# Kernel tuning notes

Hardware: AMD Instinct MI355X
Metric: run time of the kernel (lower is better)

## Reference

```python
import jax, jax.numpy as jnp
import numpy as np

N_LAYERS = 2        # f_aux_layer_num
DIM = 512           # aux_dim
HEADS = 8           # aux_attn_num
HEAD = DIM // HEADS # 64 == aux_attn_dim
FFN_H = int(DIM * 2.0)  # ffn_factor = 2.0 -> 1024
BLOCK = 64          # f_block_size n
L_BLOCKS = 32
M = BLOCK + 1       # block + router token
EPS = 1e-5
THETA = 10000.0


def rms_norm(x, w):
    return x * jax.lax.rsqrt(jnp.mean(x * x, axis=-1, keepdims=True) + EPS) * w


def rotary(x):
    # x: [b, h, s, a]; matches RotaryEmb: halves rotated with outer(t, inv_freq)
    s, a = x.shape[2], x.shape[3]
    inv_freq = (1.0 / THETA) ** (jnp.arange(0, a, 2, dtype=jnp.float32) / a)
    freqs = jnp.arange(s, dtype=jnp.float32)[:, None] * inv_freq[None, :]  # [s, a/2]
    cos, sin = jnp.cos(freqs), jnp.sin(freqs)
    x1, x2 = jnp.split(x, 2, axis=-1)
    return jnp.concatenate([x1 * cos + x2 * sin, -x1 * sin + x2 * cos], axis=-1)


def setup_inputs() -> dict:
    key = jax.random.key(0)
    ks = jax.random.split(key, 10)
    B = 2
    S = L_BLOCKS * M
    x = jax.random.normal(ks[0], (B, L_BLOCKS * BLOCK, DIM), jnp.float32)
    doc = jnp.sort(jax.random.randint(ks[1], (B, S), 0, 4, dtype=jnp.int32), axis=-1)
    w = 0.02
    return {
        "x": x,
        "doc": doc,
        "router_token": jax.random.normal(ks[2], (DIM,), jnp.float32),
        "attn_w": jax.random.normal(ks[3], (N_LAYERS, DIM, 3 * DIM), jnp.float32) * w,
        "attn_o_w": jax.random.normal(ks[4], (N_LAYERS, DIM, DIM), jnp.float32) * w,
        "ffn_up_w": jax.random.normal(ks[5], (N_LAYERS, DIM, 2 * FFN_H), jnp.float32) * w,
        "ffn_down_w": jax.random.normal(ks[6], (N_LAYERS, FFN_H, DIM), jnp.float32) * w,
        "attn_norm_w": jnp.ones((N_LAYERS, DIM), jnp.float32),
        "ffn_norm_w": jnp.ones((N_LAYERS, DIM), jnp.float32),
    }


def reference(x, doc, router_token, attn_w, attn_o_w, ffn_up_w, ffn_down_w,
              attn_norm_w, ffn_norm_w):
    b = x.shape[0]
    # insert router token after each block: [b, l, n+1, d] -> [b, s, d]
    xb = x.reshape(b, L_BLOCKS, BLOCK, DIM)
    rt = jnp.broadcast_to(router_token, (b, L_BLOCKS, 1, DIM))
    h = jnp.concatenate([xb, rt], axis=2).reshape(b, L_BLOCKS * M, DIM)
    s = h.shape[1]

    # mask_mod_1: block-causal AND same-doc
    blk = jnp.arange(s) // M
    causal = blk[:, None] >= blk[None, :]                       # [s, s]
    mask = causal[None] & (doc[:, :, None] == doc[:, None, :])  # [b, s, s]
    neg = jnp.finfo(h.dtype).min
    scale = 1.0 / jnp.sqrt(jnp.float32(HEAD))

    def split_heads(t):
        return t.reshape(b, s, HEADS, HEAD).transpose(0, 2, 1, 3)

    for i in range(N_LAYERS):
        hn = rms_norm(h, attn_norm_w[i])
        qkv = hn @ attn_w[i]                       # [b, s, 3*dim]
        q, k, v = jnp.split(qkv, 3, axis=-1)
        q, k, v = split_heads(q), split_heads(k), split_heads(v)
        q, k = rotary(q), rotary(k)
        scores = jnp.einsum('bhqa,bhka->bhqk', q, k) * scale
        scores = jnp.where(mask[:, None], scores, neg)
        attn = jax.nn.softmax(scores, axis=-1)
        o = jnp.einsum('bhqk,bhka->bhqa', attn, v)
        o = o.transpose(0, 2, 1, 3).reshape(b, s, DIM)
        h = h + o @ attn_o_w[i]
        hf = rms_norm(h, ffn_norm_w[i])
        u1, u2 = jnp.split(hf @ ffn_up_w[i], 2, axis=-1)
        h = h + (jax.nn.silu(u1) * u2) @ ffn_down_w[i]

    # keep router-token slot of each block: [b, l, d]
    return h.reshape(b, L_BLOCKS, M, DIM)[:, :, -1]
```

## Files before the change

kernel.cpp:

```cpp
#include <hip/hip_runtime.h>
#include <math.h>

#define NB 2
#define LB 32
#define BLKN 64
#define MM 65
#define SS (LB*MM)
#define DD 512
#define NH 8
#define HD 64
#define FFH 1024
#define ROWS (NB*SS)
#define WT_LS 2621440

typedef __attribute__((ext_vector_type(8))) short bf16x8;
typedef __attribute__((ext_vector_type(4))) float f32x4;

__device__ __forceinline__ unsigned short f2bf(float f) {
    union { float f; unsigned u; } v; v.f = f;
    unsigned r = (v.u + 0x7FFFu + ((v.u >> 16) & 1u)) >> 16;
    return (unsigned short)r;
}
__device__ __forceinline__ float bf2f(unsigned short u) {
    union { unsigned u; float f; } v; v.u = ((unsigned)u) << 16; return v.f;
}

__device__ __forceinline__ void gload_lds16(const unsigned short* g, unsigned short* l) {
    __builtin_amdgcn_global_load_lds((const __attribute__((address_space(1))) unsigned int*)g,
                                     (__attribute__((address_space(3))) unsigned int*)l,
                                     16, 0, 0);
}

__device__ __forceinline__ int grow_map(int r) {
    return (r >> 5) * SS + (r & 31) * MM + BLKN;
}

template <int FIRST>
__global__ __launch_bounds__(256) void rms4_k(const float* __restrict__ hsrc,
                                              const float* __restrict__ x,
                                              const float* __restrict__ rt,
                                              const float* __restrict__ w,
                                              float* __restrict__ hout,
                                              unsigned short* __restrict__ out) {
    int row = blockIdx.x * 4 + (threadIdx.x >> 6);
    int lane = threadIdx.x & 63;
    const float* sp;
    if (FIRST) {
        int s = row % SS, b = row / SS;
        int l = s / MM, j = s % MM;
        sp = (j < BLKN) ? x + ((size_t)(b * LB + l) * BLKN + j) * DD : rt;
    } else {
        sp = hsrc + (size_t)row * DD;
    }
    float4 a = *(const float4*)(sp + lane * 8);
    float4 bq = *(const float4*)(sp + lane * 8 + 4);
    float ss = a.x * a.x + a.y * a.y + a.z * a.z + a.w * a.w
             + bq.x * bq.x + bq.y * bq.y + bq.z * bq.z + bq.w * bq.w;
    #pragma unroll
    for (int off = 32; off; off >>= 1) ss += __shfl_xor(ss, off);
    float r = rsqrtf(ss * (1.0f / 512.0f) + 1e-5f);
    float4 w0 = *(const float4*)(w + lane * 8);
    float4 w1 = *(const float4*)(w + lane * 8 + 4);
    unsigned short o8[8] = {f2bf(a.x * r * w0.x), f2bf(a.y * r * w0.y),
                            f2bf(a.z * r * w0.z), f2bf(a.w * r * w0.w),
                            f2bf(bq.x * r * w1.x), f2bf(bq.y * r * w1.y),
                            f2bf(bq.z * r * w1.z), f2bf(bq.w * r * w1.w)};
    *(bf16x8*)(out + (size_t)row * DD + lane * 8) = *(const bf16x8*)o8;
    if (FIRST) {
        *(float4*)(hout + (size_t)row * DD + lane * 8) = a;
        *(float4*)(hout + (size_t)row * DD + lane * 8 + 4) = bq;
    }
}

__global__ __launch_bounds__(256) void wtrans_all_k(const float* __restrict__ attn_w,
                                                    const float* __restrict__ attn_o_w,
                                                    const float* __restrict__ up_w,
                                                    const float* __restrict__ down_w,
                                                    unsigned short* __restrict__ wt) {
    __shared__ unsigned short T[64][66];
    int wg = blockIdx.x;
    int layer = wg >= 640;
    int r = wg - layer * 640;
    const float* W; int K, N; size_t dstOff; int perm = 0;
    if (r < 192)      { W = attn_w   + (size_t)layer * 512 * 1536; K = 512;  N = 1536; dstOff = 0; }
    else if (r < 256) { W = attn_o_w + (size_t)layer * 512 * 512;  K = 512;  N = 512;  dstOff = 786432;  r -= 192; }
    else if (r < 512) { W = up_w     + (size_t)layer * 512 * 2048; K = 512;  N = 2048; dstOff = 1048576; perm = 1; r -= 256; }
    else              { W = down_w   + (size_t)layer * 1024 * 512; K = 1024; N = 512;  dstOff = 2097152; r -= 512; }
    unsigned short* dst = wt + (size_t)layer * WT_LS + dstOff;
    int ntn = N >> 6;
    int n0 = (r % ntn) * 64, k0 = (r / ntn) * 64;
    int t = threadIdx.x;
    #pragma unroll
    for (int i = 0; i < 16; ++i) {
        int e = t + i * 256;
        int rr = e >> 6, cc = e & 63;
        T[rr][cc] = f2bf(W[(size_t)(k0 + rr) * N + n0 + cc]);
    }
    __syncthreads();
    #pragma unroll
    for (int i = 0; i < 16; ++i) {
        int e = t + i * 256;
        int rr = e >> 6, cc = e & 63;
        int n = n0 + rr;
        int nr = n;
        if (perm) {
            int p = n & 1023;
            nr = ((p >> 4) << 5) | ((n >> 10) << 4) | (p & 15);
        }
        dst[(size_t)nr * K + k0 + cc] = T[cc][rr];
    }
}

template <int ADD, int OBF, int ROPE, int SILU>
__global__ __launch_bounds__(256) void gemm128_k(const unsigned short* __restrict__ A,
                                                 const unsigned short* __restrict__ Wt,
                                                 void* __restrict__ Cp,
                                                 int K, int N, int colOff) {
    __shared__ unsigned short As[128 * 64];
    __shared__ unsigned short Bs[128 * 64];
    int t = threadIdx.x;
    int lane = t & 63, wv = t >> 6;
    int wm = wv >> 1, wn = wv & 1;
    int rowBase = blockIdx.y * 128, colBase = blockIdx.x * 128;
    int c = lane & 15, g = lane >> 4;
    int sw = (c & 7) << 4;

    f32x4 acc[4][4];
    #pragma unroll
    for (int mt = 0; mt < 4; ++mt)
        #pragma unroll
        for (int nt = 0; nt < 4; ++nt) { f32x4 z = {0, 0, 0, 0}; acc[mt][nt] = z; }

    for (int k0 = 0; k0 < K; k0 += 64) {
        __syncthreads();
        #pragma unroll
        for (int i = 0; i < 4; ++i) {
            int e0 = (i * 4 + wv) * 64;
            int e = e0 + lane;
            int row = e >> 3;
            int kb = ((e & 7) << 4) ^ ((row & 7) << 4);
            int gr = rowBase + row; if (gr > ROWS - 1) gr = ROWS - 1;
            gload_lds16(A + (size_t)gr * K + k0 + (kb >> 1), &As[e0 * 8]);
        }
        #pragma unroll
        for (int i = 0; i < 4; ++i) {
            int e0 = (i * 4 + wv) * 64;
            int e = e0 + lane;
            int row = e >> 3;
            int kb = ((e & 7) << 4) ^ ((row & 7) << 4);
            gload_lds16(Wt + (size_t)(colOff + colBase + row) * K + k0 + (kb >> 1), &Bs[e0 * 8]);
        }
        __syncthreads();

        bf16x8 af[4][2], bfr[4][2];
        #pragma unroll
        for (int mt = 0; mt < 4; ++mt)
            #pragma unroll
            for (int hf = 0; hf < 2; ++hf)
                af[mt][hf] = *(const bf16x8*)
                    &As[((wm * 64 + mt * 16 + c) * 128 + ((hf * 64 + g * 16) ^ sw)) >> 1];
        #pragma unroll
        for (int nt = 0; nt < 4; ++nt)
            #pragma unroll
            for (int hf = 0; hf < 2; ++hf)
                bfr[nt][hf] = *(const bf16x8*)
                    &Bs[((wn * 64 + nt * 16 + c) * 128 + ((hf * 64 + g * 16) ^ sw)) >> 1];
        __builtin_amdgcn_s_setprio(1);
        #pragma unroll
        for (int mt = 0; mt < 4; ++mt)
            #pragma unroll
            for (int nt = 0; nt < 4; ++nt) {
                acc[mt][nt] = __builtin_amdgcn_mfma_f32_16x16x32_bf16(af[mt][0], bfr[nt][0], acc[mt][nt], 0, 0, 0);
                acc[mt][nt] = __builtin_amdgcn_mfma_f32_16x16x32_bf16(af[mt][1], bfr[nt][1], acc[mt][nt], 0, 0, 0);
            }
        __builtin_amdgcn_s_setprio(0);
    }

    if (ROPE) {
        int sec = (colOff + colBase + wn * 64) >> 9;
        if (sec < 2) {
            #pragma unroll
            for (int mt = 0; mt < 4; ++mt)
                #pragma unroll
                for (int j = 0; j < 4; ++j) {
                    int row = rowBase + wm * 64 + mt * 16 + g * 4 + j;
                    int spos = row % SS;
                    #pragma unroll
                    for (int p = 0; p < 2; ++p) {
                        float jj = (float)(c + p * 16);
                        float inv = exp2f(jj * -0.41524101186092030f);
                        float fr = (float)spos * inv;
                        float sn, cs; __sincosf(fr, &sn, &cs);
                        float a = acc[mt][p][j], bb = acc[mt][p + 2][j];
                        acc[mt][p][j] = a * cs + bb * sn;
                        acc[mt][p + 2][j] = -a * sn + bb * cs;
                    }
                }
        }
    }

    #pragma unroll
    for (int mt = 0; mt < 4; ++mt)
        #pragma unroll
        for (int j = 0; j < 4; ++j) {
            int row = rowBase + wm * 64 + mt * 16 + g * 4 + j;
            if (row >= ROWS) continue;
            if (SILU) {
                unsigned short* gr = (unsigned short*)Cp + (size_t)row * 1024;
                #pragma unroll
                for (int ntp = 0; ntp < 2; ++ntp) {
                    int npr = colBase + wn * 64 + ntp * 32;
                    int p = ((npr >> 5) << 4) + c;
                    float u1 = acc[mt][2 * ntp][j];
                    float u2 = acc[mt][2 * ntp + 1][j];
                    gr[p] = f2bf((u1 / (1.0f + __expf(-u1))) * u2);
                }
            } else {
                size_t off = (size_t)row * N + colOff + colBase + wn * 64 + c;
                if (OBF) {
                    unsigned short* cr = (unsigned short*)Cp + off;
                    #pragma unroll
                    for (int nt = 0; nt < 4; ++nt) cr[nt * 16] = f2bf(acc[mt][nt][j]);
                } else {
                    float* cr = (float*)Cp + off;
                    #pragma unroll
                    for (int nt = 0; nt < 4; ++nt) {
                        if (ADD) cr[nt * 16] += acc[mt][nt][j];
                        else     cr[nt * 16] = acc[mt][nt][j];
                    }
                }
            }
        }
}

template <int MODE, int ADD>
__global__ __launch_bounds__(256) void gemm64_k(const unsigned short* __restrict__ A,
                                                const unsigned short* __restrict__ Wt,
                                                void* __restrict__ Cp,
                                                const float* __restrict__ Hsrc,
                                                float* __restrict__ outp,
                                                int K, int N) {
    __shared__ unsigned short As[64 * 64];
    __shared__ unsigned short Bs[128 * 64];
    int t = threadIdx.x;
    int lane = t & 63, wv = t >> 6;
    int wm = wv >> 1, wn = wv & 1;
    int rowBase = blockIdx.y * 64, colBase = blockIdx.x * 128;
    int c = lane & 15, g = lane >> 4;
    int sw = (c & 7) << 4;

    f32x4 acc[2][4];
    #pragma unroll
    for (int mt = 0; mt < 2; ++mt)
        #pragma unroll
        for (int nt = 0; nt < 4; ++nt) { f32x4 z = {0, 0, 0, 0}; acc[mt][nt] = z; }

    for (int k0 = 0; k0 < K; k0 += 64) {
        __syncthreads();
        #pragma unroll
        for (int i = 0; i < 2; ++i) {
            int e0 = (i * 4 + wv) * 64;
            int e = e0 + lane;
            int row = e >> 3;
            int kb = ((e & 7) << 4) ^ ((row & 7) << 4);
            int gr = rowBase + row;
            gload_lds16(A + (size_t)gr * K + k0 + (kb >> 1), &As[e0 * 8]);
        }
        #pragma unroll
        for (int i = 0; i < 4; ++i) {
            int e0 = (i * 4 + wv) * 64;
            int e = e0 + lane;
            int row = e >> 3;
            int kb = ((e & 7) << 4) ^ ((row & 7) << 4);
            gload_lds16(Wt + (size_t)(colBase + row) * K + k0 + (kb >> 1), &Bs[e0 * 8]);
        }
        __syncthreads();

        bf16x8 af[2][2], bfr[4][2];
        #pragma unroll
        for (int mt = 0; mt < 2; ++mt)
            #pragma unroll
            for (int hf = 0; hf < 2; ++hf)
                af[mt][hf] = *(const bf16x8*)
                    &As[((wm * 32 + mt * 16 + c) * 128 + ((hf * 64 + g * 16) ^ sw)) >> 1];
        #pragma unroll
        for (int nt = 0; nt < 4; ++nt)
            #pragma unroll
            for (int hf = 0; hf < 2; ++hf)
                bfr[nt][hf] = *(const bf16x8*)
                    &Bs[((wn * 64 + nt * 16 + c) * 128 + ((hf * 64 + g * 16) ^ sw)) >> 1];
        __builtin_amdgcn_s_setprio(1);
        #pragma unroll
        for (int mt = 0; mt < 2; ++mt)
            #pragma unroll
            for (int nt = 0; nt < 4; ++nt) {
                acc[mt][nt] = __builtin_amdgcn_mfma_f32_16x16x32_bf16(af[mt][0], bfr[nt][0], acc[mt][nt], 0, 0, 0);
                acc[mt][nt] = __builtin_amdgcn_mfma_f32_16x16x32_bf16(af[mt][1], bfr[nt][1], acc[mt][nt], 0, 0, 0);
            }
        __builtin_amdgcn_s_setprio(0);
    }

    #pragma unroll
    for (int mt = 0; mt < 2; ++mt)
        #pragma unroll
        for (int j = 0; j < 4; ++j) {
            int row = rowBase + wm * 32 + mt * 16 + g * 4 + j;
            int col = colBase + wn * 64 + c;
            if (MODE == 0) {
                float* cr = (float*)Cp + (size_t)row * N + col;
                #pragma unroll
                for (int nt = 0; nt < 4; ++nt) {
                    if (ADD) cr[nt * 16] += acc[mt][nt][j];
                    else     cr[nt * 16] = acc[mt][nt][j];
                }
            } else if (MODE == 2) {
                int gr = grow_map(row);
                float* cr = (float*)Cp + (size_t)row * 512 + col;
                const float* hsr = Hsrc + (size_t)gr * 512 + col;
                #pragma unroll
                for (int nt = 0; nt < 4; ++nt) cr[nt * 16] = hsr[nt * 16] + acc[mt][nt][j];
            } else if (MODE == 3) {
                float* cr = outp + (size_t)row * 512 + col;
                const float* hsr = Hsrc + (size_t)row * 512 + col;
                #pragma unroll
                for (int nt = 0; nt < 4; ++nt) cr[nt * 16] = hsr[nt * 16] + acc[mt][nt][j];
            } else {
                unsigned short* gr = (unsigned short*)Cp + (size_t)row * 1024;
                #pragma unroll
                for (int ntp = 0; ntp < 2; ++ntp) {
                    int npr = colBase + wn * 64 + ntp * 32;
                    int p = ((npr >> 5) << 4) + c;
                    float u1 = acc[mt][2 * ntp][j];
                    float u2 = acc[mt][2 * ntp + 1][j];
                    gr[p] = f2bf((u1 / (1.0f + __expf(-u1))) * u2);
                }
            }
        }
}

#define QR 80

__global__ __launch_bounds__(320) void attn_mfma_k(const unsigned short* __restrict__ qkv,
                                                   const int* __restrict__ doc,
                                                   unsigned short* __restrict__ o) {
    __shared__ unsigned short Qs[QR * 64];
    __shared__ unsigned short Ks[2][64 * 64];
    __shared__ unsigned short Vt[2][64][72];
    __shared__ unsigned short Ps[5][16][72];
    __shared__ int docq[QR];
    __shared__ int dock[2][64];

    int idx = blockIdx.x;
    int l = 31 - (idx >> 4);
    int b = (idx >> 3) & 1;
    int h = idx & 7;
    int t = threadIdx.x;
    int lane = t & 63;
    int wv = t >> 6;

    const unsigned short* qb = qkv + (size_t)b * SS * 1536;
    int rowq0 = l * MM;
    int kmax = (l + 1) * MM;

    #pragma unroll
    for (int it = 0; it < 2; ++it) {
        int ebase = it * 320 + wv * 64;
        int e = ebase + lane;
        int row = e >> 3;
        int kb = ((e & 7) << 4) ^ ((row & 7) << 4);
        int gr = rowq0 + row; if (gr > SS - 1) gr = SS - 1;
        gload_lds16(qb + (size_t)gr * 1536 + h * 64 + (kb >> 1), &Qs[ebase * 8]);
    }
    if (t < QR) docq[t] = (t < MM) ? doc[b * SS + rowq0 + t] : -999999;

    int d0 = doc[b * SS + rowq0];
    int lo = 0, hi = rowq0;
    while (lo < hi) {
        int mid = (lo + hi) >> 1;
        if (doc[b * SS + mid] < d0) lo = mid + 1; else hi = mid;
    }
    int kts = lo >> 6;
    int nkt = (kmax + 63) >> 6;

    const int mt = wv;
    const int g = lane >> 4;
    const int c = lane & 15;
    const int sw = (c & 7) << 4;

    auto stageK = [&](int kbase, int buf) {
        int ebase = wv * 64;
        int e = ebase + lane;
        int row = e >> 3;
        int kb = ((e & 7) << 4) ^ ((row & 7) << 4);
        int kg = kbase + row; if (kg > kmax - 1) kg = kmax - 1;
        gload_lds16(qb + (size_t)kg * 1536 + 512 + h * 64 + (kb >> 1), &Ks[buf][ebase * 8]);
        if (wv < 3) {
            int eb2 = 320 + wv * 64;
            int e2 = eb2 + lane;
            int row2 = e2 >> 3;
            int kb2 = ((e2 & 7) << 4) ^ ((row2 & 7) << 4);
            int kg2 = kbase + row2; if (kg2 > kmax - 1) kg2 = kmax - 1;
            gload_lds16(qb + (size_t)kg2 * 1536 + 512 + h * 64 + (kb2 >> 1), &Ks[buf][eb2 * 8]);
        }
    };
    bf16x8 vr0, vr1; int dnx = 0;
    auto loadV = [&](int kbase) {
        int key = t & 63;
        int de = (t >> 6) * 8;
        int kg = kbase + key; if (kg > kmax - 1) kg = kmax - 1;
        vr0 = *(const bf16x8*)(qb + (size_t)kg * 1536 + 1024 + h * 64 + de);
        if (t < 192) {
            int e2 = 320 + t;
            int key2 = e2 & 63;
            int de2 = (e2 >> 6) * 8;
            int kg2 = kbase + key2; if (kg2 > kmax - 1) kg2 = kmax - 1;
            vr1 = *(const bf16x8*)(qb + (size_t)kg2 * 1536 + 1024 + h * 64 + de2);
        }
        if (t < 64) dnx = (kbase + t < kmax) ? doc[b * SS + kbase + t] : -1000000;
    };
    auto writeV = [&](int buf) {
        int key = t & 63;
        int de = (t >> 6) * 8;
        #pragma unroll
        for (int jj = 0; jj < 8; ++jj) Vt[buf][de + jj][key] = ((unsigned short*)&vr0)[jj];
        if (t < 192) {
            int e2 = 320 + t;
            int key2 = e2 & 63;
            int de2 = (e2 >> 6) * 8;
            #pragma unroll
            for (int jj = 0; jj < 8; ++jj) Vt[buf][de2 + jj][key2] = ((unsigned short*)&vr1)[jj];
        }
        if (t < 64) dock[buf][t] = dnx;
    };

    stageK(kts << 6, 0);
    loadV(kts << 6);
    writeV(0);
    __syncthreads();

    bf16x8 aq[2];
    #pragma unroll
    for (int hf = 0; hf < 2; ++hf)
        aq[hf] = *(const bf16x8*)&Qs[((mt * 16 + c) * 128 + ((hf * 64 + g * 16) ^ sw)) >> 1];
    int dq[4];
    #pragma unroll
    for (int j = 0; j < 4; ++j) dq[j] = docq[mt * 16 + g * 4 + j];

    f32x4 oacc[4];
    float m_[4], l_[4];
    #pragma unroll
    for (int nt = 0; nt < 4; ++nt) { f32x4 z = {0,0,0,0}; oacc[nt] = z; }
    #pragma unroll
    for (int j = 0; j < 4; ++j) { m_[j] = -1e30f; l_[j] = 0.0f; }

    for (int kt = kts; kt < nkt; ++kt) {
        int cur = (kt - kts) & 1;
        bool more = (kt + 1 < nkt);
        if (more) {
            stageK((kt + 1) << 6, cur ^ 1);
            loadV((kt + 1) << 6);
        }

        f32x4 s[4];
        __builtin_amdgcn_s_setprio(1);
        #pragma unroll
        for (int sub = 0; sub < 4; ++sub) {
            f32x4 acc = {0, 0, 0, 0};
            #pragma unroll
            for (int hf = 0; hf < 2; ++hf) {
                bf16x8 bk = *(const bf16x8*)
                    &Ks[cur][((sub * 16 + c) * 128 + ((hf * 64 + g * 16) ^ sw)) >> 1];
                acc = __builtin_amdgcn_mfma_f32_16x16x32_bf16(aq[hf], bk, acc, 0, 0, 0);
            }
            s[sub] = acc;
        }
        __builtin_amdgcn_s_setprio(0);
        #pragma unroll
        for (int sub = 0; sub < 4; ++sub) {
            int dk = dock[cur][sub * 16 + c];
            #pragma unroll
            for (int j = 0; j < 4; ++j)
                s[sub][j] = (dq[j] == dk) ? s[sub][j] * 0.125f : -1e30f;
        }
        float mx[4];
        #pragma unroll
        for (int j = 0; j < 4; ++j)
            mx[j] = fmaxf(fmaxf(s[0][j], s[1][j]), fmaxf(s[2][j], s[3][j]));
        #pragma unroll
        for (int off = 1; off < 16; off <<= 1)
            #pragma unroll
            for (int j = 0; j < 4; ++j) mx[j] = fmaxf(mx[j], __shfl_xor(mx[j], off));
        float mn[4], sc[4], rs[4];
        #pragma unroll
        for (int j = 0; j < 4; ++j) {
            mn[j] = fmaxf(m_[j], mx[j]);
            sc[j] = __expf(m_[j] - mn[j]);
            m_[j] = mn[j];
            rs[j] = 0.0f;
        }
        #pragma unroll
        for (int sub = 0; sub < 4; ++sub)
            #pragma unroll
            for (int j = 0; j < 4; ++j) {
                float p = __expf(s[sub][j] - mn[j]);
                rs[j] += p;
                Ps[wv][g * 4 + j][sub * 16 + c] = f2bf(p);
            }
        #pragma unroll
        for (int off = 1; off < 16; off <<= 1)
            #pragma unroll
            for (int j = 0; j < 4; ++j) rs[j] += __shfl_xor(rs[j], off);
        #pragma unroll
        for (int j = 0; j < 4; ++j) l_[j] = l_[j] * sc[j] + rs[j];
        #pragma unroll
        for (int nt = 0; nt < 4; ++nt)
            #pragma unroll
            for (int j = 0; j < 4; ++j) oacc[nt][j] *= sc[j];
        __builtin_amdgcn_s_setprio(1);
        #pragma unroll
        for (int hf = 0; hf < 2; ++hf) {
            bf16x8 af = *(const bf16x8*)&Ps[wv][c][hf * 32 + g * 8];
            #pragma unroll
            for (int nt = 0; nt < 4; ++nt) {
                bf16x8 bv = *(const bf16x8*)&Vt[cur][nt * 16 + c][hf * 32 + g * 8];
                oacc[nt] = __builtin_amdgcn_mfma_f32_16x16x32_bf16(af, bv, oacc[nt], 0, 0, 0);
            }
        }
        __builtin_amdgcn_s_setprio(0);

        if (more) writeV(cur ^ 1);
        __syncthreads();
    }

    #pragma unroll
    for (int j = 0; j < 4; ++j) {
        int row = mt * 16 + g * 4 + j;
        if (row < MM) {
            float invl = 1.0f / l_[j];
            #pragma unroll
            for (int nt = 0; nt < 4; ++nt)
                o[(size_t)(b * SS + rowq0 + row) * DD + h * 64 + nt * 16 + c] =
                    f2bf(oacc[nt][j] * invl);
        }
    }
}

__global__ __launch_bounds__(256) void rattn_k(const unsigned short* __restrict__ hnb,
                                               const unsigned short* __restrict__ qkv,
                                               const unsigned short* __restrict__ wq,
                                               const int* __restrict__ doc,
                                               unsigned short* __restrict__ obr) {
    __shared__ float hn_r[DD];
    __shared__ float qs[HD];
    __shared__ float sc[SS];
    __shared__ float red_m[4], red_s[4];
    __shared__ float pacc[4][HD];

    int idx = blockIdx.x;
    int b = idx >> 8, h = (idx >> 5) & 7, l = idx & 31;
    int t = threadIdx.x;
    int lane = t & 63, wv = t >> 6;

    const unsigned short* qb = qkv + (size_t)b * SS * 1536;
    int spos = l * MM + BLKN;
    int rowq = b * SS + spos;
    int kmax = (l + 1) * MM;

    {
        unsigned v = *(const unsigned*)(hnb + (size_t)rowq * DD + t * 2);
        hn_r[t * 2] = bf2f((unsigned short)(v & 0xffff));
        hn_r[t * 2 + 1] = bf2f((unsigned short)(v >> 16));
    }
    int dr = doc[rowq];
    int lo = 0, hi = spos;
    while (lo < hi) {
        int mid = (lo + hi) >> 1;
        if (doc[b * SS + mid] < dr) lo = mid + 1; else hi = mid;
    }
    __syncthreads();

    {
        float part = 0.0f;
        const unsigned short* wr = wq + (size_t)(h * 64 + lane) * DD + wv * 128;
        #pragma unroll
        for (int k8 = 0; k8 < 16; ++k8) {
            bf16x8 w8 = *(const bf16x8*)(wr + k8 * 8);
            #pragma unroll
            for (int j = 0; j < 8; ++j)
                part += hn_r[wv * 128 + k8 * 8 + j] * bf2f((unsigned short)w8[j]);
        }
        pacc[wv][lane] = part;
    }
    __syncthreads();
    if (wv == 0) {
        float dq = pacc[0][lane] + pacc[1][lane] + pacc[2][lane] + pacc[3][lane];
        float other = __shfl_xor(dq, 32);
        float jj = (float)(lane & 31);
        float inv = exp2f(jj * -0.41524101186092030f);
        float fr = (float)spos * inv;
        float sn, cs; __sincosf(fr, &sn, &cs);
        float q1 = (lane < 32) ? dq : other;
        float q2 = (lane < 32) ? other : dq;
        qs[lane] = (lane < 32) ? (q1 * cs + q2 * sn) : (-q1 * sn + q2 * cs);
    }
    __syncthreads();

    int dc = lane & 7, k8 = lane >> 3;
    float mx = -1e30f;
    for (int k0 = lo; k0 < kmax; k0 += 32) {
        int k = k0 + wv * 8 + k8;
        float d = 0.0f;
        if (k < kmax) {
            bf16x8 kv = *(const bf16x8*)(qb + (size_t)k * 1536 + 512 + h * 64 + dc * 8);
            #pragma unroll
            for (int j = 0; j < 8; ++j)
                d += bf2f((unsigned short)kv[j]) * qs[dc * 8 + j];
        }
        #pragma unroll
        for (int off = 1; off < 8; off <<= 1) d += __shfl_xor(d, off);
        if (k < kmax) {
            float s = d * 0.125f;
            if (dc == 0) sc[k] = s;
            mx = fmaxf(mx, s);
        }
    }
    #pragma unroll
    for (int off = 32; off; off >>= 1) mx = fmaxf(mx, __shfl_xor(mx, off));
    if (lane == 0) red_m[wv] = mx;
    __syncthreads();
    mx = fmaxf(fmaxf(red_m[0], red_m[1]), fmaxf(red_m[2], red_m[3]));

    float sum = 0.0f;
    for (int k = lo + t; k < kmax; k += 256) {
        float p = __expf(sc[k] - mx);
        sc[k] = p;
        sum += p;
    }
    #pragma unroll
    for (int off = 32; off; off >>= 1) sum += __shfl_xor(sum, off);
    if (lane == 0) red_s[wv] = sum;
    __syncthreads();
    sum = red_s[0] + red_s[1] + red_s[2] + red_s[3];

    float acc = 0.0f;
    #pragma unroll 4
    for (int k = lo + wv; k < kmax; k += 4) {
        float vv = bf2f(qb[(size_t)k * 1536 + 1024 + h * 64 + lane]);
        acc += sc[k] * vv;
    }
    pacc[wv][lane] = acc;
    __syncthreads();
    if (wv == 0) {
        float o = (pacc[0][lane] + pacc[1][lane] + pacc[2][lane] + pacc[3][lane]) / sum;
        obr[(size_t)(b * LB + l) * DD + h * 64 + lane] = f2bf(o);
    }
}

extern "C" void kernel_launch(void* const* d_in, const int* in_sizes, int n_in,
                              void* d_out, int out_size, void* d_ws, size_t ws_size,
                              hipStream_t stream) {
    const float* x           = (const float*)d_in[0];
    const int*   doc         = (const int*)d_in[1];
    const float* rt          = (const float*)d_in[2];
    const float* attn_w      = (const float*)d_in[3];
    const float* attn_o_w    = (const float*)d_in[4];
    const float* ffn_up_w    = (const float*)d_in[5];
    const float* ffn_down_w  = (const float*)d_in[6];
    const float* attn_norm_w = (const float*)d_in[7];
    const float* ffn_norm_w  = (const float*)d_in[8];
    float* out = (float*)d_out;

    float* h = (float*)d_ws;
    unsigned short* qkvb = (unsigned short*)(h + (size_t)ROWS * 512);
    unsigned short* wt   = qkvb + (size_t)ROWS * 1536;
    unsigned short* hnb  = wt + (size_t)2 * WT_LS;
    unsigned short* ob   = hnb + (size_t)ROWS * 512;
    unsigned short* gb   = ob + (size_t)ROWS * 512;
    unsigned short* obr  = gb + (size_t)ROWS * 1024;
    unsigned short* hnr  = obr + 64 * 512;
    unsigned short* gbr  = hnr + 64 * 512;
    float* hr = (float*)(gbr + 64 * 1024);

    wtrans_all_k<<<1280, 256, 0, stream>>>(attn_w, attn_o_w, ffn_up_w, ffn_down_w, wt);

    rms4_k<1><<<ROWS / 4, 256, 0, stream>>>(h, x, rt, attn_norm_w, h, hnb);
    gemm128_k<0, 1, 1, 0><<<dim3(12, 33), 256, 0, stream>>>(hnb, wt, qkvb, 512, 1536, 0);
    attn_mfma_k<<<512, 320, 0, stream>>>(qkvb, doc, ob);
    gemm64_k<0, 1><<<dim3(4, 65), 256, 0, stream>>>(ob, wt + 786432, h, nullptr, nullptr, 512, 512);
    rms4_k<0><<<ROWS / 4, 256, 0, stream>>>(h, x, rt, ffn_norm_w, h, hnb);
    gemm128_k<0, 0, 0, 1><<<dim3(16, 33), 256, 0, stream>>>(hnb, wt + 1048576, gb, 512, 2048, 0);
    gemm64_k<0, 1><<<dim3(4, 65), 256, 0, stream>>>(gb, wt + 2097152, h, nullptr, nullptr, 1024, 512);

    unsigned short* wl = wt + (size_t)WT_LS;
    rms4_k<0><<<ROWS / 4, 256, 0, stream>>>(h, x, rt, attn_norm_w + 512, h, hnb);
    gemm128_k<0, 1, 1, 0><<<dim3(8, 33), 256, 0, stream>>>(hnb, wl, qkvb, 512, 1536, 512);
    rattn_k<<<512, 256, 0, stream>>>(hnb, qkvb, wl, doc, obr);
    gemm64_k<2, 0><<<dim3(4, 1), 256, 0, stream>>>(obr, wl + 786432, hr, h, nullptr, 512, 512);
    rms4_k<0><<<16, 256, 0, stream>>>(hr, x, rt, ffn_norm_w + 512, nullptr, hnr);
    gemm64_k<4, 0><<<dim3(16, 1), 256, 0, stream>>>(hnr, wl + 1048576, gbr, nullptr, nullptr, 512, 2048);
    gemm64_k<3, 0><<<dim3(4, 1), 256, 0, stream>>>(gbr, wl + 2097152, nullptr, hr, out, 1024, 512);
}
```

Baseline: 198.9 us.

## Store residual stream in bf16 and unroll router attention PV loop

The fp32 residual buffer h becomes bf16 throughout, in the RMS norm kernels, the GEMM residual-add epilogues and the router path, which halves residual read/write traffic. The attention kernel's block index mapping changes for the second half of the grid, and the router attention's PV accumulation uses four independent accumulators for more ILP. Keeping the residual in bf16 drops precision on the accumulated stream and adds rounding at each residual add, so accuracy could drift.

After: 202.5 us. Within noise of the previous version (+1.8%).

```diff
diff --git a/kernel.cpp b/kernel.cpp
--- a/kernel.cpp
+++ b/kernel.cpp
@@ -36,39 +36,46 @@
 }
 
 template <int FIRST>
-__global__ __launch_bounds__(256) void rms4_k(const float* __restrict__ hsrc,
+__global__ __launch_bounds__(256) void rms4_k(const unsigned short* __restrict__ hsrc,
                                               const float* __restrict__ x,
                                               const float* __restrict__ rt,
                                               const float* __restrict__ w,
-                                              float* __restrict__ hout,
+                                              unsigned short* __restrict__ hout,
                                               unsigned short* __restrict__ out) {
     int row = blockIdx.x * 4 + (threadIdx.x >> 6);
     int lane = threadIdx.x & 63;
-    const float* sp;
+    float v[8];
     if (FIRST) {
         int s = row % SS, b = row / SS;
         int l = s / MM, j = s % MM;
-        sp = (j < BLKN) ? x + ((size_t)(b * LB + l) * BLKN + j) * DD : rt;
+        const float* sp = (j < BLKN) ? x + ((size_t)(b * LB + l) * BLKN + j) * DD : rt;
+        float4 a = *(const float4*)(sp + lane * 8);
+        float4 bq = *(const float4*)(sp + lane * 8 + 4);
+        v[0] = a.x; v[1] = a.y; v[2] = a.z; v[3] = a.w;
+        v[4] = bq.x; v[5] = bq.y; v[6] = bq.z; v[7] = bq.w;
     } else {
-        sp = hsrc + (size_t)row * DD;
-    }
-    float4 a = *(const float4*)(sp + lane * 8);
-    float4 bq = *(const float4*)(sp + lane * 8 + 4);
-    float ss = a.x * a.x + a.y * a.y + a.z * a.z + a.w * a.w
-             + bq.x * bq.x + bq.y * bq.y + bq.z * bq.z + bq.w * bq.w;
+        bf16x8 h8 = *(const bf16x8*)(hsrc + (size_t)row * DD + lane * 8);
+        #pragma unroll
+        for (int j = 0; j < 8; ++j) v[j] = bf2f((unsigned short)h8[j]);
+    }
+    float ss = 0.0f;
+    #pragma unroll
+    for (int j = 0; j < 8; ++j) ss += v[j] * v[j];
     #pragma unroll
     for (int off = 32; off; off >>= 1) ss += __shfl_xor(ss, off);
     float r = rsqrtf(ss * (1.0f / 512.0f) + 1e-5f);
     float4 w0 = *(const float4*)(w + lane * 8);
     float4 w1 = *(const float4*)(w + lane * 8 + 4);
-    unsigned short o8[8] = {f2bf(a.x * r * w0.x), f2bf(a.y * r * w0.y),
-                            f2bf(a.z * r * w0.z), f2bf(a.w * r * w0.w),
-                            f2bf(bq.x * r * w1.x), f2bf(bq.y * r * w1.y),
-                            f2bf(bq.z * r * w1.z), f2bf(bq.w * r * w1.w)};
+    float wv[8] = {w0.x, w0.y, w0.z, w0.w, w1.x, w1.y, w1.z, w1.w};
+    unsigned short o8[8];
+    #pragma unroll
+    for (int j = 0; j < 8; ++j) o8[j] = f2bf(v[j] * r * wv[j]);
     *(bf16x8*)(out + (size_t)row * DD + lane * 8) = *(const bf16x8*)o8;
     if (FIRST) {
-        *(float4*)(hout + (size_t)row * DD + lane * 8) = a;
-        *(float4*)(hout + (size_t)row * DD + lane * 8 + 4) = bq;
+        unsigned short h8[8];
+        #pragma unroll
+        for (int j = 0; j < 8; ++j) h8[j] = f2bf(v[j]);
+        *(bf16x8*)(hout + (size_t)row * DD + lane * 8) = *(const bf16x8*)h8;
     }
 }
 
@@ -237,7 +244,7 @@
 __global__ __launch_bounds__(256) void gemm64_k(const unsigned short* __restrict__ A,
                                                 const unsigned short* __restrict__ Wt,
                                                 void* __restrict__ Cp,
-                                                const float* __restrict__ Hsrc,
+                                                const unsigned short* __restrict__ Hsrc,
                                                 float* __restrict__ outp,
                                                 int K, int N) {
     __shared__ unsigned short As[64 * 64];
@@ -307,23 +314,28 @@
             int row = rowBase + wm * 32 + mt * 16 + g * 4 + j;
             int col = colBase + wn * 64 + c;
             if (MODE == 0) {
-                float* cr = (float*)Cp + (size_t)row * N + col;
-                #pragma unroll
-                for (int nt = 0; nt < 4; ++nt) {
-                    if (ADD) cr[nt * 16] += acc[mt][nt][j];
-                    else     cr[nt * 16] = acc[mt][nt][j];
+                if (ADD) {
+                    unsigned short* cr = (unsigned short*)Cp + (size_t)row * N + col;
+                    #pragma unroll
+                    for (int nt = 0; nt < 4; ++nt)
+                        cr[nt * 16] = f2bf(bf2f(cr[nt * 16]) + acc[mt][nt][j]);
+                } else {
+                    float* cr = (float*)Cp + (size_t)row * N + col;
+                    #pragma unroll
+                    for (int nt = 0; nt < 4; ++nt) cr[nt * 16] = acc[mt][nt][j];
                 }
             } else if (MODE == 2) {
                 int gr = grow_map(row);
-                float* cr = (float*)Cp + (size_t)row * 512 + col;
-                const float* hsr = Hsrc + (size_t)gr * 512 + col;
+                unsigned short* cr = (unsigned short*)Cp + (size_t)row * 512 + col;
+                const unsigned short* hsr = Hsrc + (size_t)gr * 512 + col;
                 #pragma unroll
-                for (int nt = 0; nt < 4; ++nt) cr[nt * 16] = hsr[nt * 16] + acc[mt][nt][j];
+                for (int nt = 0; nt < 4; ++nt)
+                    cr[nt * 16] = f2bf(bf2f(hsr[nt * 16]) + acc[mt][nt][j]);
             } else if (MODE == 3) {
                 float* cr = outp + (size_t)row * 512 + col;
-                const float* hsr = Hsrc + (size_t)row * 512 + col;
+                const unsigned short* hsr = Hsrc + (size_t)row * 512 + col;
                 #pragma unroll
-                for (int nt = 0; nt < 4; ++nt) cr[nt * 16] = hsr[nt * 16] + acc[mt][nt][j];
+                for (int nt = 0; nt < 4; ++nt) cr[nt * 16] = bf2f(hsr[nt * 16]) + acc[mt][nt][j];
             } else {
                 unsigned short* gr = (unsigned short*)Cp + (size_t)row * 1024;
                 #pragma unroll
@@ -351,7 +363,7 @@
     __shared__ int dock[2][64];
 
     int idx = blockIdx.x;
-    int l = 31 - (idx >> 4);
+    int l = (idx < 256) ? (31 - (idx >> 4)) : ((idx - 256) >> 4);
     int b = (idx >> 3) & 1;
     int h = idx & 7;
     int t = threadIdx.x;
@@ -642,13 +654,17 @@
     __syncthreads();
     sum = red_s[0] + red_s[1] + red_s[2] + red_s[3];
 
-    float acc = 0.0f;
-    #pragma unroll 4
-    for (int k = lo + wv; k < kmax; k += 4) {
-        float vv = bf2f(qb[(size_t)k * 1536 + 1024 + h * 64 + lane]);
-        acc += sc[k] * vv;
-    }
-    pacc[wv][lane] = acc;
+    float a0 = 0, a1 = 0, a2 = 0, a3 = 0;
+    int k = lo + wv;
+    for (; k + 12 < kmax; k += 16) {
+        a0 += sc[k]      * bf2f(qb[(size_t)k * 1536 + 1024 + h * 64 + lane]);
+        a1 += sc[k + 4]  * bf2f(qb[(size_t)(k + 4) * 1536 + 1024 + h * 64 + lane]);
+        a2 += sc[k + 8]  * bf2f(qb[(size_t)(k + 8) * 1536 + 1024 + h * 64 + lane]);
+        a3 += sc[k + 12] * bf2f(qb[(size_t)(k + 12) * 1536 + 1024 + h * 64 + lane]);
+    }
+    for (; k < kmax; k += 4)
+        a0 += sc[k] * bf2f(qb[(size_t)k * 1536 + 1024 + h * 64 + lane]);
+    pacc[wv][lane] = (a0 + a1) + (a2 + a3);
     __syncthreads();
     if (wv == 0) {
         float o = (pacc[0][lane] + pacc[1][lane] + pacc[2][lane] + pacc[3][lane]) / sum;
@@ -670,8 +686,8 @@
     const float* ffn_norm_w  = (const float*)d_in[8];
     float* out = (float*)d_out;
 
-    float* h = (float*)d_ws;
-    unsigned short* qkvb = (unsigned short*)(h + (size_t)ROWS * 512);
+    unsigned short* hb   = (unsigned short*)d_ws;
+    unsigned short* qkvb = hb + (size_t)ROWS * 512;
     unsigned short* wt   = qkvb + (size_t)ROWS * 1536;
     unsigned short* hnb  = wt + (size_t)2 * WT_LS;
     unsigned short* ob   = hnb + (size_t)ROWS * 512;
@@ -679,23 +695,23 @@
     unsigned short* obr  = gb + (size_t)ROWS * 1024;
     unsigned short* hnr  = obr + 64 * 512;
     unsigned short* gbr  = hnr + 64 * 512;
-    float* hr = (float*)(gbr + 64 * 1024);
+    unsigned short* hr   = gbr + 64 * 1024;
 
     wtrans_all_k<<<1280, 256, 0, stream>>>(attn_w, attn_o_w, ffn_up_w, ffn_down_w, wt);
 
-    rms4_k<1><<<ROWS / 4, 256, 0, stream>>>(h, x, rt, attn_norm_w, h, hnb);
+    rms4_k<1><<<ROWS / 4, 256, 0, stream>>>(hb, x, rt, attn_norm_w, hb, hnb);
     gemm128_k<0, 1, 1, 0><<<dim3(12, 33), 256, 0, stream>>>(hnb, wt, qkvb, 512, 1536, 0);
     attn_mfma_k<<<512, 320, 0, stream>>>(qkvb, doc, ob);
-    gemm64_k<0, 1><<<dim3(4, 65), 256, 0, stream>>>(ob, wt + 786432, h, nullptr, nullptr, 512, 512);
-    rms4_k<0><<<ROWS / 4, 256, 0, stream>>>(h, x, rt, ffn_norm_w, h, hnb);
+    gemm64_k<0, 1><<<dim3(4, 65), 256, 0, stream>>>(ob, wt + 786432, hb, nullptr, nullptr, 512, 512);
+    rms4_k<0><<<ROWS / 4, 256, 0, stream>>>(hb, x, rt, ffn_norm_w, nullptr, hnb);
     gemm128_k<0, 0, 0, 1><<<dim3(16, 33), 256, 0, stream>>>(hnb, wt + 1048576, gb, 512, 2048, 0);
-    gemm64_k<0, 1><<<dim3(4, 65), 256, 0, stream>>>(gb, wt + 2097152, h, nullptr, nullptr, 1024, 512);
+    gemm64_k<0, 1><<<dim3(4, 65), 256, 0, stream>>>(gb, wt + 2097152, hb, nullptr, nullptr, 1024, 512);
 
     unsigned short* wl = wt + (size_t)WT_LS;
-    rms4_k<0><<<ROWS / 4, 256, 0, stream>>>(h, x, rt, attn_norm_w + 512, h, hnb);
+    rms4_k<0><<<ROWS / 4, 256, 0, stream>>>(hb, x, rt, attn_norm_w + 512, nullptr, hnb);
     gemm128_k<0, 1, 1, 0><<<dim3(8, 33), 256, 0, stream>>>(hnb, wl, qkvb, 512, 1536, 512);
     rattn_k<<<512, 256, 0, stream>>>(hnb, qkvb, wl, doc, obr);
-    gemm64_k<2, 0><<<dim3(4, 1), 256, 0, stream>>>(obr, wl + 786432, hr, h, nullptr, 512, 512);
+    gemm64_k<2, 0><<<dim3(4, 1), 256, 0, stream>>>(obr, wl + 786432, hr, hb, nullptr, 512, 512);
     rms4_k<0><<<16, 256, 0, stream>>>(hr, x, rt, ffn_norm_w + 512, nullptr, hnr);
     gemm64_k<4, 0><<<dim3(16, 1), 256, 0, stream>>>(hnr, wl + 1048576, gbr, nullptr, nullptr, 512, 2048);
     gemm64_k<3, 0><<<dim3(4, 1), 256, 0, stream>>>(gbr, wl + 2097152, nullptr, hr, out, 1024, 512);
```
